# Optimization experiments

Hardware: AMD Instinct MI355X
Metric: run time of the kernel (lower is better)

The kernel has to match this reference:

```python
import jax, jax.numpy as jnp
import numpy as np

B, N, D, H, DH = 2, 4096, 256, 8, 64   # batch, nodes, dim, heads, dim_head
INNER = H * DH
POLY_K = 3  # polynomial order -> coeffs [H, POLY_K+1]
LN_EPS = 1e-5


def setup_inputs() -> dict:
    key = jax.random.key(0)
    ks = jax.random.split(key, 8)
    s = 0.02
    return {
        "x": jax.random.normal(ks[0], (B, N, D), dtype=jnp.float32),
        "Wq": jax.random.normal(ks[1], (D, INNER), dtype=jnp.float32) * s,
        "Wk": jax.random.normal(ks[2], (D, INNER), dtype=jnp.float32) * s,
        "Wv": jax.random.normal(ks[3], (D, INNER), dtype=jnp.float32) * s,
        "Wo": jax.random.normal(ks[4], (INNER, D), dtype=jnp.float32) * s,
        "gamma": jnp.ones((DH,), dtype=jnp.float32),
        "beta": jnp.zeros((DH,), dtype=jnp.float32),
        "coeffs": jax.random.normal(ks[5], (H, POLY_K + 1), dtype=jnp.float32) * 0.5,
    }


def reference(x, Wq, Wk, Wv, Wo, gamma, beta, coeffs):
    b, n, d = x.shape
    h, dh = coeffs.shape[0], gamma.shape[0]
    # --- graph estimator: per-head softmax adjacency A = softmax(QK^T/sqrt(dh)) ---
    q = (x @ Wq).reshape(b, n, h, dh).transpose(0, 2, 1, 3)  # bhnd
    k = (x @ Wk).reshape(b, n, h, dh).transpose(0, 2, 1, 3)  # bhnd
    scale = jax.lax.rsqrt(jnp.asarray(dh, x.dtype))
    A = jax.nn.softmax(jnp.einsum('bhnd,bhmd->bhnm', q, k) * scale, axis=-1)
    # --- value projection + per-head LayerNorm over dim_head ---
    v = (x @ Wv).reshape(b, n, h, dh)
    mu = v.mean(axis=-1, keepdims=True)
    var = ((v - mu) ** 2).mean(axis=-1, keepdims=True)
    v = (v - mu) * jax.lax.rsqrt(var + LN_EPS) * gamma + beta
    v = v.transpose(0, 2, 1, 3)  # bhnd
    # --- polynomial graph filter: y = sum_k c[h,k] * A^k v ---
    y = coeffs[None, :, 0, None, None] * v
    t = v
    for kk in range(1, coeffs.shape[1]):
        t = jnp.einsum('bhnm,bhmd->bhnd', A, t)
        y = y + coeffs[None, :, kk, None, None] * t
    # --- merge heads + output projection ---
    merged = y.transpose(0, 2, 1, 3).reshape(b, n, h * dh)
    return merged @ Wo
```

## Files before the change

kernel.cpp:

```cpp
#include <hip/hip_runtime.h>
#include <stdint.h>

#define B_ 2
#define N_ 4096
#define D_ 256
#define H_ 8
#define DH_ 64
#define INNER_ 512
#define NBH 16
#define PAD 72
#define FPAD 80

typedef unsigned short ushort_t;
typedef __attribute__((ext_vector_type(8))) short short8;
typedef __attribute__((ext_vector_type(4))) float float4v;
typedef __attribute__((ext_vector_type(4))) unsigned short ushort4v;
typedef __attribute__((ext_vector_type(4))) unsigned int uint4v;

__device__ __forceinline__ ushort_t f2bf(float f) {
    union { float f; unsigned int u; } v; v.f = f;
    unsigned int r = v.u + 0x7FFFu + ((v.u >> 16) & 1u);
    return (ushort_t)(r >> 16);
}
__device__ __forceinline__ float bf2f(ushort_t u) {
    union { unsigned int u; float f; } v; v.u = ((unsigned int)u) << 16;
    return v.f;
}
__device__ __forceinline__ unsigned char f2fp8s(float f) {
    union { float f; unsigned int u; } v; v.f = f;
    unsigned int s = (v.u >> 24) & 0x80u;
    v.u &= 0x7FFFFFFFu;
    float a = v.f;
    if (a >= 448.f) return (unsigned char)(s | 0x7E);
    if (a < 0.015625f) {
        int m = (int)(a * 512.f + 0.5f);
        return (unsigned char)(s | (unsigned)m);
    }
    unsigned int u = v.u + 0x7FFFFu + ((v.u >> 20) & 1u);
    return (unsigned char)(s | (((u >> 20) & 0x7FF) - 960));
}
__device__ __forceinline__ float fexp2(float x) {
    float r;
    asm volatile("v_exp_f32 %0, %1\n\ts_nop 0" : "=v"(r) : "v"(x));
    return r;
}

__global__ __launch_bounds__(256) void prep_kernel(
    const float* __restrict__ x, const float* __restrict__ Wq,
    const float* __restrict__ Wk, const float* __restrict__ Wv,
    const float* __restrict__ Wo,
    ushort_t* __restrict__ xb, ushort_t* __restrict__ WqkvT,
    ushort_t* __restrict__ WoT) {
    int idx = blockIdx.x * 256 + threadIdx.x;
    const int total_x = B_ * N_ * D_;
    const int total_wqkv = 3 * INNER_ * D_;
    const int total_wo = D_ * INNER_;
    if (idx < total_x) { xb[idx] = f2bf(x[idx]); return; }
    idx -= total_x;
    if (idx < total_wqkv) {
        int n = idx >> 8, k = idx & 255;
        int which = n >> 9, nn = n & 511;
        const float* W = (which == 0) ? Wq : ((which == 1) ? Wk : Wv);
        WqkvT[idx] = f2bf(W[k * INNER_ + nn]);
        return;
    }
    idx -= total_wqkv;
    if (idx < total_wo) {
        int c = idx >> 9, k = idx & 511;
        WoT[idx] = f2bf(Wo[k * D_ + c]);
    }
}

__global__ __launch_bounds__(256) void proj_gemm(
    const ushort_t* __restrict__ xb, const ushort_t* __restrict__ WqkvT,
    ushort_t* __restrict__ Qb, ushort_t* __restrict__ Kb,
    ushort_t* __restrict__ Vb) {
    __shared__ ushort_t As[128][PAD];
    __shared__ ushort_t Bs[128][PAD];
    int bid = blockIdx.x;
    int tileN = bid % 12, tileM = bid / 12;
    int tid = threadIdx.x;
    int w = tid >> 6, lane = tid & 63, q = lane >> 4, r = lane & 15;
    int wr = (w & 1) * 64, wc = (w >> 1) * 64;
    float4v acc[4][4];
    for (int i = 0; i < 4; i++)
        for (int j = 0; j < 4; j++)
            for (int e = 0; e < 4; e++) acc[i][j][e] = 0.f;

    for (int k0 = 0; k0 < 256; k0 += 64) {
        for (int it = 0; it < 4; it++) {
            int idx = tid + it * 256;
            int row = idx >> 3, kc = (idx & 7) * 8;
            *(short8*)&As[row][kc] =
                *(const short8*)&xb[(size_t)(tileM * 128 + row) * 256 + k0 + kc];
            *(short8*)&Bs[row][kc] =
                *(const short8*)&WqkvT[(size_t)(tileN * 128 + row) * 256 + k0 + kc];
        }
        __syncthreads();
        for (int kk = 0; kk < 64; kk += 32) {
            short8 a[4], b[4];
            for (int mi = 0; mi < 4; mi++)
                a[mi] = *(const short8*)&As[wr + mi * 16 + r][kk + q * 8];
            for (int ni = 0; ni < 4; ni++)
                b[ni] = *(const short8*)&Bs[wc + ni * 16 + r][kk + q * 8];
            for (int mi = 0; mi < 4; mi++)
                for (int ni = 0; ni < 4; ni++)
                    acc[mi][ni] = __builtin_amdgcn_mfma_f32_16x16x32_bf16(
                        a[mi], b[ni], acc[mi][ni], 0, 0, 0);
        }
        __syncthreads();
    }
    for (int mi = 0; mi < 4; mi++)
        for (int ni = 0; ni < 4; ni++)
            for (int reg = 0; reg < 4; reg++) {
                int grow = tileM * 128 + wr + mi * 16 + q * 4 + reg;
                int gcol = tileN * 128 + wc + ni * 16 + r;
                float v = acc[mi][ni][reg];
                int which = gcol >> 9, inner = gcol & 511;
                int h = inner >> 6, d = inner & 63;
                int b = grow >> 12, n = grow & 4095;
                size_t off = (((size_t)(b * H_ + h)) * N_ + n) * DH_ + d;
                if (which == 0) Qb[off] = f2bf(v * 0.18033688011112042f);
                else if (which == 1) Kb[off] = f2bf(v);
                else Vb[off] = f2bf(v);
            }
}

__global__ __launch_bounds__(256) void ln_kernel(
    const ushort_t* __restrict__ Vb, const float* __restrict__ gamma,
    const float* __restrict__ beta, const float* __restrict__ coeffs,
    unsigned char* __restrict__ t0T, float* __restrict__ y) {
    int tid = threadIdx.x;
    int wave = tid >> 6, lane = tid & 63;
    size_t row = (size_t)blockIdx.x * 4 + wave;
    int bh = (int)(row >> 12), n = (int)(row & 4095);
    int h = bh & 7;
    float v = bf2f(Vb[row * 64 + lane]);
    float s = v;
    for (int m = 32; m >= 1; m >>= 1) s += __shfl_xor(s, m, 64);
    float mu = s * (1.f / 64.f);
    float dv = v - mu;
    float s2 = dv * dv;
    for (int m = 32; m >= 1; m >>= 1) s2 += __shfl_xor(s2, m, 64);
    float var = s2 * (1.f / 64.f);
    float vln = dv * rsqrtf(var + 1e-5f) * gamma[lane] + beta[lane];
    float c0 = coeffs[h * 4 + 0];
    y[row * 64 + lane] = c0 * vln;
    t0T[((size_t)bh * 64 + lane) * 4096 + n] = f2fp8s(vln);
}


#define MFB(a, b, c) __builtin_amdgcn_mfma_f32_16x16x32_bf16(a, b, c, 0, 0, 0)
#define MFP(a, b, c) __builtin_amdgcn_mfma_f32_16x16x32_fp8_fp8(a, b, c, 0, 0, 0)

__device__ __forceinline__ long pk8(float4v x, float4v y) {
    int d0 = __builtin_amdgcn_cvt_pk_fp8_f32(fexp2(x[0]), fexp2(x[1]), 0, false);
    d0 = __builtin_amdgcn_cvt_pk_fp8_f32(fexp2(x[2]), fexp2(x[3]), d0, true);
    int d1 = __builtin_amdgcn_cvt_pk_fp8_f32(fexp2(y[0]), fexp2(y[1]), 0, false);
    d1 = __builtin_amdgcn_cvt_pk_fp8_f32(fexp2(y[2]), fexp2(y[3]), d1, true);
    return (long)(((unsigned long)(unsigned int)d1 << 32) | (unsigned int)d0);
}

#define WGBAR()                                                \
    do {                                                       \
        asm volatile("s_waitcnt lgkmcnt(0)" ::: "memory");     \
        __builtin_amdgcn_sched_barrier(0);                     \
        __builtin_amdgcn_s_barrier();                          \
        __builtin_amdgcn_sched_barrier(0);                     \
    } while (0)

#define COMPUTE32(KsX, TsX)                                                     \
    {                                                                           \
        short8 a0, a1;                                                          \
        float4v s00, s10, s20, s30, s01, s11, s21, s31;                         \
        a0 = *(const short8*)&KsX[r][q * 8];                                    \
        a1 = *(const short8*)&KsX[r][32 + q * 8];                               \
        s00 = MFB(a1, qf1, MFB(a0, qf0, zf));                                   \
        s01 = MFB(a1, qf3, MFB(a0, qf2, zf));                                   \
        a0 = *(const short8*)&KsX[16 + r][q * 8];                               \
        a1 = *(const short8*)&KsX[16 + r][32 + q * 8];                          \
        s10 = MFB(a1, qf1, MFB(a0, qf0, zf));                                   \
        s11 = MFB(a1, qf3, MFB(a0, qf2, zf));                                   \
        a0 = *(const short8*)&KsX[32 + r][q * 8];                               \
        a1 = *(const short8*)&KsX[32 + r][32 + q * 8];                          \
        s20 = MFB(a1, qf1, MFB(a0, qf0, zf));                                   \
        s21 = MFB(a1, qf3, MFB(a0, qf2, zf));                                   \
        a0 = *(const short8*)&KsX[48 + r][q * 8];                               \
        a1 = *(const short8*)&KsX[48 + r][32 + q * 8];                          \
        s30 = MFB(a1, qf1, MFB(a0, qf0, zf));                                   \
        s31 = MFB(a1, qf3, MFB(a0, qf2, zf));                                   \
        long eA0 = pk8(s00, s10), eB0 = pk8(s20, s30);                          \
        long eA1 = pk8(s01, s11), eB1 = pk8(s21, s31);                          \
        long b0 = *(const long*)&TsX[r][q * 8];                                 \
        long b1 = *(const long*)&TsX[16 + r][q * 8];                            \
        long b2 = *(const long*)&TsX[32 + r][q * 8];                            \
        long b3 = *(const long*)&TsX[48 + r][q * 8];                            \
        acc0[0] = MFP(eA0, b0, acc0[0]); acc1[0] = MFP(eA1, b0, acc1[0]);       \
        acc0[1] = MFP(eA0, b1, acc0[1]); acc1[1] = MFP(eA1, b1, acc1[1]);       \
        acc0[2] = MFP(eA0, b2, acc0[2]); acc1[2] = MFP(eA1, b2, acc1[2]);       \
        acc0[3] = MFP(eA0, b3, acc0[3]); acc1[3] = MFP(eA1, b3, acc1[3]);       \
        accs0 = MFP(eA0, bones, accs0);  accs1 = MFP(eA1, bones, accs1);        \
        b0 = *(const long*)&TsX[r][32 + q * 8];                                 \
        b1 = *(const long*)&TsX[16 + r][32 + q * 8];                            \
        b2 = *(const long*)&TsX[32 + r][32 + q * 8];                            \
        b3 = *(const long*)&TsX[48 + r][32 + q * 8];                            \
        acc0[0] = MFP(eB0, b0, acc0[0]); acc1[0] = MFP(eB1, b0, acc1[0]);       \
        acc0[1] = MFP(eB0, b1, acc0[1]); acc1[1] = MFP(eB1, b1, acc1[1]);       \
        acc0[2] = MFP(eB0, b2, acc0[2]); acc1[2] = MFP(eB1, b2, acc1[2]);       \
        acc0[3] = MFP(eB0, b3, acc0[3]); acc1[3] = MFP(eB1, b3, acc1[3]);       \
        accs0 = MFP(eB0, bones, accs0);  accs1 = MFP(eB1, bones, accs1);        \
    }

__global__ __launch_bounds__(512, 4) void poly_pass(
    const ushort_t* __restrict__ Qb, const ushort_t* __restrict__ Kb,
    const unsigned char* __restrict__ tinT, float* __restrict__ y,
    unsigned char* __restrict__ toutT, const float* __restrict__ coeffs,
    int kidx, int write_t) {
    __shared__ char smem[57344];
    typedef ushort_t KsArr[64][PAD];
    typedef unsigned char TsArr[64][FPAD];
    KsArr* Ks0 = (KsArr*)smem;
    KsArr* Ks1 = (KsArr*)(smem + 18432);
    TsArr* Ts0 = (TsArr*)(smem + 36864);
    TsArr* Ts1 = (TsArr*)(smem + 47104);

    int bid0 = blockIdx.x;
    int bid = ((bid0 & 7) << 6) | (bid0 >> 3);
    int bh = bid >> 5, ti = bid & 31;
    const ushort_t* Q = Qb + (size_t)bh * N_ * 64;
    const ushort_t* K = Kb + (size_t)bh * N_ * 64;
    const unsigned char* tin = tinT + (size_t)bh * 64 * N_;
    int tid = threadIdx.x, w = tid >> 6, lane = tid & 63, q = lane >> 4, r = lane & 15;
    int half = w >> 2, wsub = w & 3;
    const float4v zf = {0.f, 0.f, 0.f, 0.f};

    const ushort_t* qp = Q + (size_t)(ti * 128 + wsub * 32 + r) * 64 + q * 8;
    short8 qf0 = *(const short8*)qp;
    short8 qf1 = *(const short8*)(qp + 32);
    short8 qf2 = *(const short8*)(qp + 16 * 64);
    short8 qf3 = *(const short8*)(qp + 16 * 64 + 32);

    float4v acc0[4], acc1[4], accs0, accs1;
    for (int e = 0; e < 4; e++) { accs0[e] = 0.f; accs1[e] = 0.f; }
    for (int j = 0; j < 4; j++)
        for (int e = 0; e < 4; e++) { acc0[j][e] = 0.f; acc1[j][e] = 0.f; }
    const long bones = 0x3838383838383838L;

    int tl = tid & 255;
    int krow = tl >> 2, kpart = (tl & 3) * 16;
    int Lrow = (krow & 32) + ((krow & 4) << 2) + (krow & 3) + ((krow >> 3) & 3) * 4;
    const ushort_t* kp = K + (size_t)(half * 2048 + krow) * 64 + kpart;
    int srow = tl >> 2, scol = (tl & 3) * 16;
    const unsigned char* tp = tin + (size_t)srow * 4096 + half * 2048 + scol;

    {
        uint4v ka = *(const uint4v*)kp;
        uint4v kb = *(const uint4v*)(kp + 8);
        uint4v tv = *(const uint4v*)tp;
        *(uint4v*)&Ks0[half][Lrow][kpart] = ka;
        *(uint4v*)&Ks0[half][Lrow][kpart + 8] = kb;
        *(uint4v*)&Ts0[half][srow][scol] = tv;
    }
    uint4v pka = *(const uint4v*)(kp + 4096);
    uint4v pkb = *(const uint4v*)(kp + 4096 + 8);
    uint4v pt  = *(const uint4v*)(tp + 64);
    const ushort_t* kpl = kp + 2 * 4096;
    const unsigned char* tpl = tp + 2 * 64;
    WGBAR();

    for (int it = 0; it < 32; it += 2) {
        *(uint4v*)&Ks1[half][Lrow][kpart] = pka;
        *(uint4v*)&Ks1[half][Lrow][kpart + 8] = pkb;
        *(uint4v*)&Ts1[half][srow][scol] = pt;
        pka = *(const uint4v*)kpl;
        pkb = *(const uint4v*)(kpl + 8);
        pt  = *(const uint4v*)tpl;
        kpl += 4096; tpl += 64;
        COMPUTE32(Ks0[half], Ts0[half]);
        WGBAR();
        *(uint4v*)&Ks0[half][Lrow][kpart] = pka;
        *(uint4v*)&Ks0[half][Lrow][kpart + 8] = pkb;
        *(uint4v*)&Ts0[half][srow][scol] = pt;
        pka = *(const uint4v*)kpl;
        pkb = *(const uint4v*)(kpl + 8);
        pt  = *(const uint4v*)tpl;
        kpl += 4096; tpl += 64;
        COMPUTE32(Ks1[half], Ts1[half]);
        WGBAR();
    }

    float* ULDS = (float*)smem;
    unsigned char (*TT)[144] = (unsigned char(*)[144])(smem + 40960);

    if (half == 1) {
        float* ub = ULDS + (size_t)(wsub * 64 + lane) * 40;
#pragma unroll
        for (int j = 0; j < 4; j++) {
            *(float4v*)(ub + j * 4) = acc0[j];
            *(float4v*)(ub + 16 + j * 4) = acc1[j];
        }
        *(float4v*)(ub + 32) = accs0;
        *(float4v*)(ub + 36) = accs1;
    }
    WGBAR();
    if (half == 0) {
        const float* ub = ULDS + (size_t)(wsub * 64 + lane) * 40;
#pragma unroll
        for (int j = 0; j < 4; j++) {
            acc0[j] += *(const float4v*)(ub + j * 4);
            acc1[j] += *(const float4v*)(ub + 16 + j * 4);
        }
        accs0 += *(const float4v*)(ub + 32);
        accs1 += *(const float4v*)(ub + 36);

        int h = bh & 7;
        float ck = coeffs[h * 4 + kidx];
        float rinv0[4], rinv1[4];
#pragma unroll
        for (int reg = 0; reg < 4; reg++) {
            rinv0[reg] = 1.f / accs0[reg];
            rinv1[reg] = 1.f / accs1[reg];
        }
        float tv0[4][4], tv1[4][4];
#pragma unroll
        for (int ni = 0; ni < 4; ni++)
#pragma unroll
            for (int reg = 0; reg < 4; reg++) {
                tv0[ni][reg] = acc0[ni][reg] * rinv0[reg];
                tv1[ni][reg] = acc1[ni][reg] * rinv1[reg];
            }
#pragma unroll
        for (int reg = 0; reg < 4; reg++) {
            int il = wsub * 32 + q * 4 + reg;
            float* yp0 = y + ((size_t)bh * N_ + (size_t)ti * 128 + il) * 64;
            float* yp1 = yp0 + 16 * 64;
#pragma unroll
            for (int ni = 0; ni < 4; ni++) {
                yp0[ni * 16 + r] += ck * tv0[ni][reg];
                yp1[ni * 16 + r] += ck * tv1[ni][reg];
            }
        }
        if (write_t) {
#pragma unroll
            for (int ni = 0; ni < 4; ni++) {
                int p0 = __builtin_amdgcn_cvt_pk_fp8_f32(tv0[ni][0], tv0[ni][1], 0, false);
                p0 = __builtin_amdgcn_cvt_pk_fp8_f32(tv0[ni][2], tv0[ni][3], p0, true);
                *(unsigned int*)&TT[ni * 16 + r][wsub * 32 + q * 4] = (unsigned int)p0;
                int p1 = __builtin_amdgcn_cvt_pk_fp8_f32(tv1[ni][0], tv1[ni][1], 0, false);
                p1 = __builtin_amdgcn_cvt_pk_fp8_f32(tv1[ni][2], tv1[ni][3], p1, true);
                *(unsigned int*)&TT[ni * 16 + r][wsub * 32 + 16 + q * 4] = (unsigned int)p1;
            }
        }
    }
    if (write_t) {
        WGBAR();
        int drow = tid >> 3, dcol = (tid & 7) * 16;
        uint4v vv = *(const uint4v*)&TT[drow][dcol];
        *(uint4v*)&toutT[(size_t)bh * 64 * N_ + (size_t)drow * N_ + ti * 128 + dcol] = vv;
    }
}

__global__ __launch_bounds__(256) void out_gemm(
    const float* __restrict__ y, const ushort_t* __restrict__ WoT,
    float* __restrict__ out) {
    __shared__ ushort_t As[128][PAD];
    __shared__ ushort_t Bs[64][PAD];
    int bid = blockIdx.x;
    int tileN = bid & 3, tileM = bid >> 2;
    int tid = threadIdx.x, w = tid >> 6, lane = tid & 63, q = lane >> 4, r = lane & 15;
    int wr = w * 32;
    float4v acc[2][4];
    for (int i = 0; i < 2; i++)
        for (int j = 0; j < 4; j++)
            for (int e = 0; e < 4; e++) acc[i][j][e] = 0.f;

    for (int k0 = 0; k0 < 512; k0 += 64) {
        int h = k0 >> 6;
        for (int it = 0; it < 8; it++) {
            int idx = tid + it * 256;
            int row = idx >> 4, kc = (idx & 15) * 4;
            int grow = tileM * 128 + row;
            int b = grow >> 12, n = grow & 4095;
            const float4* src =
                (const float4*)&y[(((size_t)(b * H_ + h)) * N_ + n) * 64 + kc];
            float4 v = *src;
            ushort4v pv;
            pv[0] = f2bf(v.x); pv[1] = f2bf(v.y); pv[2] = f2bf(v.z); pv[3] = f2bf(v.w);
            *(ushort4v*)&As[row][kc] = pv;
        }
        for (int it = 0; it < 2; it++) {
            int idx = tid + it * 256;
            int row = idx >> 3, kc = (idx & 7) * 8;
            *(short8*)&Bs[row][kc] =
                *(const short8*)&WoT[(size_t)(tileN * 64 + row) * 512 + k0 + kc];
        }
        __syncthreads();
        for (int kk = 0; kk < 64; kk += 32) {
            short8 a[2], b[4];
            a[0] = *(const short8*)&As[wr + r][kk + q * 8];
            a[1] = *(const short8*)&As[wr + 16 + r][kk + q * 8];
            for (int ni = 0; ni < 4; ni++)
                b[ni] = *(const short8*)&Bs[ni * 16 + r][kk + q * 8];
            for (int mi = 0; mi < 2; mi++)
                for (int ni = 0; ni < 4; ni++)
                    acc[mi][ni] = __builtin_amdgcn_mfma_f32_16x16x32_bf16(
                        a[mi], b[ni], acc[mi][ni], 0, 0, 0);
        }
        __syncthreads();
    }
    for (int mi = 0; mi < 2; mi++)
        for (int reg = 0; reg < 4; reg++) {
            int grow = tileM * 128 + wr + mi * 16 + q * 4 + reg;
            for (int ni = 0; ni < 4; ni++) {
                int gcol = tileN * 64 + ni * 16 + r;
                out[(size_t)grow * 256 + gcol] = acc[mi][ni][reg];
            }
        }
}

extern "C" void kernel_launch(void* const* d_in, const int* in_sizes, int n_in,
                              void* d_out, int out_size, void* d_ws, size_t ws_size,
                              hipStream_t stream) {
    const float* x      = (const float*)d_in[0];
    const float* Wq     = (const float*)d_in[1];
    const float* Wk     = (const float*)d_in[2];
    const float* Wv     = (const float*)d_in[3];
    const float* Wo     = (const float*)d_in[4];
    const float* gamma  = (const float*)d_in[5];
    const float* beta   = (const float*)d_in[6];
    const float* coeffs = (const float*)d_in[7];
    float* out = (float*)d_out;

    char* ws = (char*)d_ws;
    size_t off = 0;
    auto alloc = [&](size_t bytes) -> void* {
        void* p = ws + off;
        off += (bytes + 255) & ~(size_t)255;
        return p;
    };
    ushort_t* xb    = (ushort_t*)alloc((size_t)B_ * N_ * D_ * 2);
    ushort_t* WqkvT = (ushort_t*)alloc((size_t)3 * INNER_ * D_ * 2);
    ushort_t* WoT   = (ushort_t*)alloc((size_t)D_ * INNER_ * 2);
    ushort_t* Qb    = (ushort_t*)alloc((size_t)NBH * N_ * DH_ * 2);
    ushort_t* Kb    = (ushort_t*)alloc((size_t)NBH * N_ * DH_ * 2);
    ushort_t* Vb    = (ushort_t*)alloc((size_t)NBH * N_ * DH_ * 2);
    unsigned char* t0T = (unsigned char*)alloc((size_t)NBH * DH_ * N_);
    unsigned char* t1T = (unsigned char*)alloc((size_t)NBH * DH_ * N_);
    float*    y     = (float*)alloc((size_t)NBH * N_ * DH_ * 4);

    const int prep_total = B_ * N_ * D_ + 3 * INNER_ * D_ + D_ * INNER_;
    prep_kernel<<<(prep_total + 255) / 256, 256, 0, stream>>>(
        x, Wq, Wk, Wv, Wo, xb, WqkvT, WoT);
    proj_gemm<<<768, 256, 0, stream>>>(xb, WqkvT, Qb, Kb, Vb);
    ln_kernel<<<(NBH * N_) / 4, 256, 0, stream>>>(Vb, gamma, beta, coeffs, t0T, y);

    poly_pass<<<NBH * 32, 512, 0, stream>>>(Qb, Kb, t0T, y, t1T, coeffs, 1, 1);
    poly_pass<<<NBH * 32, 512, 0, stream>>>(Qb, Kb, t1T, y, t0T, coeffs, 2, 1);
    poly_pass<<<NBH * 32, 512, 0, stream>>>(Qb, Kb, t0T, y, t1T, coeffs, 3, 0);

    out_gemm<<<256, 256, 0, stream>>>(y, WoT, out);
}
```

Baseline: 361.2 us.

## Double poly_pass query tile to 256 rows per block to reuse K/T tiles

Each poly_pass block now handles 256 query rows (64 per wave) instead of 128. Each K and T tile loaded into LDS therefore feeds twice as many MFMAs, which halves the number of blocks and the global and LDS traffic per unit of work. The cost is roughly double the accumulator registers per wave, so launch bounds drop to 2 waves-per-EU, and only 256 blocks are launched, which may leave the 256 CUs underfilled. LDS padding changes and the split-K reduction across wave halves now runs in two rounds to fit the larger accumulators.

```diff
diff --git a/kernel.cpp b/kernel.cpp
--- a/kernel.cpp
+++ b/kernel.cpp
@@ -9,7 +9,8 @@
 #define INNER_ 512
 #define NBH 16
 #define PAD 72
-#define FPAD 80
+#define KPAD 74
+#define FPAD 88
 
 typedef unsigned short ushort_t;
 typedef __attribute__((ext_vector_type(8))) short short8;
@@ -169,64 +170,91 @@
         __builtin_amdgcn_sched_barrier(0);                     \
     } while (0)
 
-#define COMPUTE32(KsX, TsX)                                                     \
+#define COMPUTE64(KsX, TsX)                                                     \
     {                                                                           \
         short8 a0, a1;                                                          \
-        float4v s00, s10, s20, s30, s01, s11, s21, s31;                         \
-        a0 = *(const short8*)&KsX[r][q * 8];                                    \
-        a1 = *(const short8*)&KsX[r][32 + q * 8];                               \
-        s00 = MFB(a1, qf1, MFB(a0, qf0, zf));                                   \
-        s01 = MFB(a1, qf3, MFB(a0, qf2, zf));                                   \
-        a0 = *(const short8*)&KsX[16 + r][q * 8];                               \
-        a1 = *(const short8*)&KsX[16 + r][32 + q * 8];                          \
-        s10 = MFB(a1, qf1, MFB(a0, qf0, zf));                                   \
-        s11 = MFB(a1, qf3, MFB(a0, qf2, zf));                                   \
-        a0 = *(const short8*)&KsX[32 + r][q * 8];                               \
-        a1 = *(const short8*)&KsX[32 + r][32 + q * 8];                          \
-        s20 = MFB(a1, qf1, MFB(a0, qf0, zf));                                   \
-        s21 = MFB(a1, qf3, MFB(a0, qf2, zf));                                   \
-        a0 = *(const short8*)&KsX[48 + r][q * 8];                               \
-        a1 = *(const short8*)&KsX[48 + r][32 + q * 8];                          \
-        s30 = MFB(a1, qf1, MFB(a0, qf0, zf));                                   \
-        s31 = MFB(a1, qf3, MFB(a0, qf2, zf));                                   \
-        long eA0 = pk8(s00, s10), eB0 = pk8(s20, s30);                          \
-        long eA1 = pk8(s01, s11), eB1 = pk8(s21, s31);                          \
-        long b0 = *(const long*)&TsX[r][q * 8];                                 \
-        long b1 = *(const long*)&TsX[16 + r][q * 8];                            \
-        long b2 = *(const long*)&TsX[32 + r][q * 8];                            \
-        long b3 = *(const long*)&TsX[48 + r][q * 8];                            \
-        acc0[0] = MFP(eA0, b0, acc0[0]); acc1[0] = MFP(eA1, b0, acc1[0]);       \
-        acc0[1] = MFP(eA0, b1, acc0[1]); acc1[1] = MFP(eA1, b1, acc1[1]);       \
-        acc0[2] = MFP(eA0, b2, acc0[2]); acc1[2] = MFP(eA1, b2, acc1[2]);       \
-        acc0[3] = MFP(eA0, b3, acc0[3]); acc1[3] = MFP(eA1, b3, acc1[3]);       \
-        accs0 = MFP(eA0, bones, accs0);  accs1 = MFP(eA1, bones, accs1);        \
-        b0 = *(const long*)&TsX[r][32 + q * 8];                                 \
-        b1 = *(const long*)&TsX[16 + r][32 + q * 8];                            \
-        b2 = *(const long*)&TsX[32 + r][32 + q * 8];                            \
-        b3 = *(const long*)&TsX[48 + r][32 + q * 8];                            \
-        acc0[0] = MFP(eB0, b0, acc0[0]); acc1[0] = MFP(eB1, b0, acc1[0]);       \
-        acc0[1] = MFP(eB0, b1, acc0[1]); acc1[1] = MFP(eB1, b1, acc1[1]);       \
-        acc0[2] = MFP(eB0, b2, acc0[2]); acc1[2] = MFP(eB1, b2, acc1[2]);       \
-        acc0[3] = MFP(eB0, b3, acc0[3]); acc1[3] = MFP(eB1, b3, acc1[3]);       \
-        accs0 = MFP(eB0, bones, accs0);  accs1 = MFP(eB1, bones, accs1);        \
-    }
-
-__global__ __launch_bounds__(512, 4) void poly_pass(
+        long e00, e01, e02, e03, e10, e11, e12, e13;                            \
+        {                                                                       \
+            float4v sA0, sA1, sA2, sA3, sB0, sB1, sB2, sB3;                     \
+            a0 = *(const short8*)&KsX[r][q * 8];                                \
+            a1 = *(const short8*)&KsX[r][32 + q * 8];                           \
+            sA0 = MFB(a1, qf0b, MFB(a0, qf0a, zf));                             \
+            sA1 = MFB(a1, qf1b, MFB(a0, qf1a, zf));                             \
+            sA2 = MFB(a1, qf2b, MFB(a0, qf2a, zf));                             \
+            sA3 = MFB(a1, qf3b, MFB(a0, qf3a, zf));                             \
+            a0 = *(const short8*)&KsX[16 + r][q * 8];                           \
+            a1 = *(const short8*)&KsX[16 + r][32 + q * 8];                      \
+            sB0 = MFB(a1, qf0b, MFB(a0, qf0a, zf));                             \
+            sB1 = MFB(a1, qf1b, MFB(a0, qf1a, zf));                             \
+            sB2 = MFB(a1, qf2b, MFB(a0, qf2a, zf));                             \
+            sB3 = MFB(a1, qf3b, MFB(a0, qf3a, zf));                             \
+            e00 = pk8(sA0, sB0); e01 = pk8(sA1, sB1);                           \
+            e02 = pk8(sA2, sB2); e03 = pk8(sA3, sB3);                           \
+        }                                                                       \
+        {                                                                       \
+            float4v sA0, sA1, sA2, sA3, sB0, sB1, sB2, sB3;                     \
+            a0 = *(const short8*)&KsX[32 + r][q * 8];                           \
+            a1 = *(const short8*)&KsX[32 + r][32 + q * 8];                      \
+            sA0 = MFB(a1, qf0b, MFB(a0, qf0a, zf));                             \
+            sA1 = MFB(a1, qf1b, MFB(a0, qf1a, zf));                             \
+            sA2 = MFB(a1, qf2b, MFB(a0, qf2a, zf));                             \
+            sA3 = MFB(a1, qf3b, MFB(a0, qf3a, zf));                             \
+            a0 = *(const short8*)&KsX[48 + r][q * 8];                           \
+            a1 = *(const short8*)&KsX[48 + r][32 + q * 8];                      \
+            sB0 = MFB(a1, qf0b, MFB(a0, qf0a, zf));                             \
+            sB1 = MFB(a1, qf1b, MFB(a0, qf1a, zf));                             \
+            sB2 = MFB(a1, qf2b, MFB(a0, qf2a, zf));                             \
+            sB3 = MFB(a1, qf3b, MFB(a0, qf3a, zf));                             \
+            e10 = pk8(sA0, sB0); e11 = pk8(sA1, sB1);                           \
+            e12 = pk8(sA2, sB2); e13 = pk8(sA3, sB3);                           \
+        }                                                                       \
+        long tb;                                                                \
+        tb = *(const long*)&TsX[r][q * 8];                                      \
+        acc0[0] = MFP(e00, tb, acc0[0]); acc1[0] = MFP(e01, tb, acc1[0]);       \
+        acc2[0] = MFP(e02, tb, acc2[0]); acc3[0] = MFP(e03, tb, acc3[0]);       \
+        tb = *(const long*)&TsX[r][32 + q * 8];                                 \
+        acc0[0] = MFP(e10, tb, acc0[0]); acc1[0] = MFP(e11, tb, acc1[0]);       \
+        acc2[0] = MFP(e12, tb, acc2[0]); acc3[0] = MFP(e13, tb, acc3[0]);       \
+        tb = *(const long*)&TsX[16 + r][q * 8];                                 \
+        acc0[1] = MFP(e00, tb, acc0[1]); acc1[1] = MFP(e01, tb, acc1[1]);       \
+        acc2[1] = MFP(e02, tb, acc2[1]); acc3[1] = MFP(e03, tb, acc3[1]);       \
+        tb = *(const long*)&TsX[16 + r][32 + q * 8];                            \
+        acc0[1] = MFP(e10, tb, acc0[1]); acc1[1] = MFP(e11, tb, acc1[1]);       \
+        acc2[1] = MFP(e12, tb, acc2[1]); acc3[1] = MFP(e13, tb, acc3[1]);       \
+        tb = *(const long*)&TsX[32 + r][q * 8];                                 \
+        acc0[2] = MFP(e00, tb, acc0[2]); acc1[2] = MFP(e01, tb, acc1[2]);       \
+        acc2[2] = MFP(e02, tb, acc2[2]); acc3[2] = MFP(e03, tb, acc3[2]);       \
+        tb = *(const long*)&TsX[32 + r][32 + q * 8];                            \
+        acc0[2] = MFP(e10, tb, acc0[2]); acc1[2] = MFP(e11, tb, acc1[2]);       \
+        acc2[2] = MFP(e12, tb, acc2[2]); acc3[2] = MFP(e13, tb, acc3[2]);       \
+        tb = *(const long*)&TsX[48 + r][q * 8];                                 \
+        acc0[3] = MFP(e00, tb, acc0[3]); acc1[3] = MFP(e01, tb, acc1[3]);       \
+        acc2[3] = MFP(e02, tb, acc2[3]); acc3[3] = MFP(e03, tb, acc3[3]);       \
+        tb = *(const long*)&TsX[48 + r][32 + q * 8];                            \
+        acc0[3] = MFP(e10, tb, acc0[3]); acc1[3] = MFP(e11, tb, acc1[3]);       \
+        acc2[3] = MFP(e12, tb, acc2[3]); acc3[3] = MFP(e13, tb, acc3[3]);       \
+        accs0 = MFP(e00, bones, accs0); accs0 = MFP(e10, bones, accs0);         \
+        accs1 = MFP(e01, bones, accs1); accs1 = MFP(e11, bones, accs1);         \
+        accs2 = MFP(e02, bones, accs2); accs2 = MFP(e12, bones, accs2);         \
+        accs3 = MFP(e03, bones, accs3); accs3 = MFP(e13, bones, accs3);         \
+    }
+
+__global__ __launch_bounds__(512, 2) void poly_pass(
     const ushort_t* __restrict__ Qb, const ushort_t* __restrict__ Kb,
     const unsigned char* __restrict__ tinT, float* __restrict__ y,
     unsigned char* __restrict__ toutT, const float* __restrict__ coeffs,
     int kidx, int write_t) {
-    __shared__ char smem[57344];
-    typedef ushort_t KsArr[64][PAD];
+    __shared__ char smem[60416];
+    typedef ushort_t KsArr[64][KPAD];
     typedef unsigned char TsArr[64][FPAD];
     KsArr* Ks0 = (KsArr*)smem;
-    KsArr* Ks1 = (KsArr*)(smem + 18432);
-    TsArr* Ts0 = (TsArr*)(smem + 36864);
-    TsArr* Ts1 = (TsArr*)(smem + 47104);
+    KsArr* Ks1 = (KsArr*)(smem + 18944);
+    TsArr* Ts0 = (TsArr*)(smem + 37888);
+    TsArr* Ts1 = (TsArr*)(smem + 49152);
 
     int bid0 = blockIdx.x;
-    int bid = ((bid0 & 7) << 6) | (bid0 >> 3);
-    int bh = bid >> 5, ti = bid & 31;
+    int bid = ((bid0 & 7) << 5) | (bid0 >> 3);
+    int bh = bid >> 4, ti = bid & 15;
     const ushort_t* Q = Qb + (size_t)bh * N_ * 64;
     const ushort_t* K = Kb + (size_t)bh * N_ * 64;
     const unsigned char* tin = tinT + (size_t)bh * 64 * N_;
@@ -234,16 +262,20 @@
     int half = w >> 2, wsub = w & 3;
     const float4v zf = {0.f, 0.f, 0.f, 0.f};
 
-    const ushort_t* qp = Q + (size_t)(ti * 128 + wsub * 32 + r) * 64 + q * 8;
-    short8 qf0 = *(const short8*)qp;
-    short8 qf1 = *(const short8*)(qp + 32);
-    short8 qf2 = *(const short8*)(qp + 16 * 64);
-    short8 qf3 = *(const short8*)(qp + 16 * 64 + 32);
-
-    float4v acc0[4], acc1[4], accs0, accs1;
-    for (int e = 0; e < 4; e++) { accs0[e] = 0.f; accs1[e] = 0.f; }
+    const ushort_t* qp = Q + (size_t)(ti * 256 + wsub * 64 + r) * 64 + q * 8;
+    short8 qf0a = *(const short8*)qp;
+    short8 qf0b = *(const short8*)(qp + 32);
+    short8 qf1a = *(const short8*)(qp + 16 * 64);
+    short8 qf1b = *(const short8*)(qp + 16 * 64 + 32);
+    short8 qf2a = *(const short8*)(qp + 32 * 64);
+    short8 qf2b = *(const short8*)(qp + 32 * 64 + 32);
+    short8 qf3a = *(const short8*)(qp + 48 * 64);
+    short8 qf3b = *(const short8*)(qp + 48 * 64 + 32);
+
+    float4v acc0[4], acc1[4], acc2[4], acc3[4], accs0, accs1, accs2, accs3;
+    for (int e = 0; e < 4; e++) { accs0[e] = 0.f; accs1[e] = 0.f; accs2[e] = 0.f; accs3[e] = 0.f; }
     for (int j = 0; j < 4; j++)
-        for (int e = 0; e < 4; e++) { acc0[j][e] = 0.f; acc1[j][e] = 0.f; }
+        for (int e = 0; e < 4; e++) { acc0[j][e] = 0.f; acc1[j][e] = 0.f; acc2[j][e] = 0.f; acc3[j][e] = 0.f; }
     const long bones = 0x3838383838383838L;
 
     int tl = tid & 255;
@@ -276,7 +308,7 @@
         pkb = *(const uint4v*)(kpl + 8);
         pt  = *(const uint4v*)tpl;
         kpl += 4096; tpl += 64;
-        COMPUTE32(Ks0[half], Ts0[half]);
+        COMPUTE64(Ks0[half], Ts0[half]);
         WGBAR();
         *(uint4v*)&Ks0[half][Lrow][kpart] = pka;
         *(uint4v*)&Ks0[half][Lrow][kpart + 8] = pkb;
@@ -285,78 +317,105 @@
         pkb = *(const uint4v*)(kpl + 8);
         pt  = *(const uint4v*)tpl;
         kpl += 4096; tpl += 64;
-        COMPUTE32(Ks1[half], Ts1[half]);
+        COMPUTE64(Ks1[half], Ts1[half]);
         WGBAR();
     }
 
     float* ULDS = (float*)smem;
-    unsigned char (*TT)[144] = (unsigned char(*)[144])(smem + 40960);
-
-    if (half == 1) {
-        float* ub = ULDS + (size_t)(wsub * 64 + lane) * 40;
-#pragma unroll
-        for (int j = 0; j < 4; j++) {
-            *(float4v*)(ub + j * 4) = acc0[j];
-            *(float4v*)(ub + 16 + j * 4) = acc1[j];
-        }
-        *(float4v*)(ub + 32) = accs0;
-        *(float4v*)(ub + 36) = accs1;
-    }
-    WGBAR();
+    for (int rr = 0; rr < 2; rr++) {
+        if (half == 1 && (wsub >> 1) == rr) {
+            float* ub = ULDS + (size_t)((wsub & 1) * 64 + lane) * 84;
+            *(float4v*)(ub + 0)  = acc0[0]; *(float4v*)(ub + 4)  = acc0[1];
+            *(float4v*)(ub + 8)  = acc0[2]; *(float4v*)(ub + 12) = acc0[3];
+            *(float4v*)(ub + 16) = acc1[0]; *(float4v*)(ub + 20) = acc1[1];
+            *(float4v*)(ub + 24) = acc1[2]; *(float4v*)(ub + 28) = acc1[3];
+            *(float4v*)(ub + 32) = acc2[0]; *(float4v*)(ub + 36) = acc2[1];
+            *(float4v*)(ub + 40) = acc2[2]; *(float4v*)(ub + 44) = acc2[3];
+            *(float4v*)(ub + 48) = acc3[0]; *(float4v*)(ub + 52) = acc3[1];
+            *(float4v*)(ub + 56) = acc3[2]; *(float4v*)(ub + 60) = acc3[3];
+            *(float4v*)(ub + 64) = accs0;   *(float4v*)(ub + 68) = accs1;
+            *(float4v*)(ub + 72) = accs2;   *(float4v*)(ub + 76) = accs3;
+        }
+        WGBAR();
+        if (half == 0 && (wsub >> 1) == rr) {
+            const float* ub = ULDS + (size_t)((wsub & 1) * 64 + lane) * 84;
+            acc0[0] += *(const float4v*)(ub + 0);  acc0[1] += *(const float4v*)(ub + 4);
+            acc0[2] += *(const float4v*)(ub + 8);  acc0[3] += *(const float4v*)(ub + 12);
+            acc1[0] += *(const float4v*)(ub + 16); acc1[1] += *(const float4v*)(ub + 20);
+            acc1[2] += *(const float4v*)(ub + 24); acc1[3] += *(const float4v*)(ub + 28);
+            acc2[0] += *(const float4v*)(ub + 32); acc2[1] += *(const float4v*)(ub + 36);
+            acc2[2] += *(const float4v*)(ub + 40); acc2[3] += *(const float4v*)(ub + 44);
+            acc3[0] += *(const float4v*)(ub + 48); acc3[1] += *(const float4v*)(ub + 52);
+            acc3[2] += *(const float4v*)(ub + 56); acc3[3] += *(const float4v*)(ub + 60);
+            accs0 += *(const float4v*)(ub + 64);   accs1 += *(const float4v*)(ub + 68);
+            accs2 += *(const float4v*)(ub + 72);   accs3 += *(const float4v*)(ub + 76);
+        }
+        WGBAR();
+    }
+
+    unsigned char (*TT)[272] = (unsigned char(*)[272])smem;
     if (half == 0) {
-        const float* ub = ULDS + (size_t)(wsub * 64 + lane) * 40;
-#pragma unroll
-        for (int j = 0; j < 4; j++) {
-            acc0[j] += *(const float4v*)(ub + j * 4);
-            acc1[j] += *(const float4v*)(ub + 16 + j * 4);
-        }
-        accs0 += *(const float4v*)(ub + 32);
-        accs1 += *(const float4v*)(ub + 36);
-
         int h = bh & 7;
         float ck = coeffs[h * 4 + kidx];
-        float rinv0[4], rinv1[4];
+        float r0[4], r1[4], r2[4], r3[4];
 #pragma unroll
         for (int reg = 0; reg < 4; reg++) {
-            rinv0[reg] = 1.f / accs0[reg];
-            rinv1[reg] = 1.f / accs1[reg];
-        }
-        float tv0[4][4], tv1[4][4];
+            r0[reg] = 1.f / accs0[reg]; r1[reg] = 1.f / accs1[reg];
+            r2[reg] = 1.f / accs2[reg]; r3[reg] = 1.f / accs3[reg];
+        }
+        float tv0[4][4], tv1[4][4], tv2[4][4], tv3[4][4];
 #pragma unroll
-        for (int ni = 0; ni < 4; ni++)
+        for (int dg = 0; dg < 4; dg++)
 #pragma unroll
             for (int reg = 0; reg < 4; reg++) {
-                tv0[ni][reg] = acc0[ni][reg] * rinv0[reg];
-                tv1[ni][reg] = acc1[ni][reg] * rinv1[reg];
+                tv0[dg][reg] = acc0[dg][reg] * r0[reg];
+                tv1[dg][reg] = acc1[dg][reg] * r1[reg];
+                tv2[dg][reg] = acc2[dg][reg] * r2[reg];
+                tv3[dg][reg] = acc3[dg][reg] * r3[reg];
             }
 #pragma unroll
         for (int reg = 0; reg < 4; reg++) {
-            int il = wsub * 32 + q * 4 + reg;
-            float* yp0 = y + ((size_t)bh * N_ + (size_t)ti * 128 + il) * 64;
-            float* yp1 = yp0 + 16 * 64;
+            size_t ibase = (size_t)bh * N_ + (size_t)ti * 256 + wsub * 64 + q * 4 + reg;
+            float* yp0 = y + (ibase + 0)  * 64;
+            float* yp1 = y + (ibase + 16) * 64;
+            float* yp2 = y + (ibase + 32) * 64;
+            float* yp3 = y + (ibase + 48) * 64;
 #pragma unroll
-            for (int ni = 0; ni < 4; ni++) {
-                yp0[ni * 16 + r] += ck * tv0[ni][reg];
-                yp1[ni * 16 + r] += ck * tv1[ni][reg];
+            for (int dg = 0; dg < 4; dg++) {
+                yp0[dg * 16 + r] += ck * tv0[dg][reg];
+                yp1[dg * 16 + r] += ck * tv1[dg][reg];
+                yp2[dg * 16 + r] += ck * tv2[dg][reg];
+                yp3[dg * 16 + r] += ck * tv3[dg][reg];
             }
         }
         if (write_t) {
 #pragma unroll
-            for (int ni = 0; ni < 4; ni++) {
-                int p0 = __builtin_amdgcn_cvt_pk_fp8_f32(tv0[ni][0], tv0[ni][1], 0, false);
-                p0 = __builtin_amdgcn_cvt_pk_fp8_f32(tv0[ni][2], tv0[ni][3], p0, true);
-                *(unsigned int*)&TT[ni * 16 + r][wsub * 32 + q * 4] = (unsigned int)p0;
-                int p1 = __builtin_amdgcn_cvt_pk_fp8_f32(tv1[ni][0], tv1[ni][1], 0, false);
-                p1 = __builtin_amdgcn_cvt_pk_fp8_f32(tv1[ni][2], tv1[ni][3], p1, true);
-                *(unsigned int*)&TT[ni * 16 + r][wsub * 32 + 16 + q * 4] = (unsigned int)p1;
+            for (int dg = 0; dg < 4; dg++) {
+                int p;
+                p = __builtin_amdgcn_cvt_pk_fp8_f32(tv0[dg][0], tv0[dg][1], 0, false);
+                p = __builtin_amdgcn_cvt_pk_fp8_f32(tv0[dg][2], tv0[dg][3], p, true);
+                *(unsigned int*)&TT[dg * 16 + r][wsub * 64 + q * 4] = (unsigned int)p;
+                p = __builtin_amdgcn_cvt_pk_fp8_f32(tv1[dg][0], tv1[dg][1], 0, false);
+                p = __builtin_amdgcn_cvt_pk_fp8_f32(tv1[dg][2], tv1[dg][3], p, true);
+                *(unsigned int*)&TT[dg * 16 + r][wsub * 64 + 16 + q * 4] = (unsigned int)p;
+                p = __builtin_amdgcn_cvt_pk_fp8_f32(tv2[dg][0], tv2[dg][1], 0, false);
+                p = __builtin_amdgcn_cvt_pk_fp8_f32(tv2[dg][2], tv2[dg][3], p, true);
+                *(unsigned int*)&TT[dg * 16 + r][wsub * 64 + 32 + q * 4] = (unsigned int)p;
+                p = __builtin_amdgcn_cvt_pk_fp8_f32(tv3[dg][0], tv3[dg][1], 0, false);
+                p = __builtin_amdgcn_cvt_pk_fp8_f32(tv3[dg][2], tv3[dg][3], p, true);
+                *(unsigned int*)&TT[dg * 16 + r][wsub * 64 + 48 + q * 4] = (unsigned int)p;
             }
         }
     }
     if (write_t) {
         WGBAR();
-        int drow = tid >> 3, dcol = (tid & 7) * 16;
-        uint4v vv = *(const uint4v*)&TT[drow][dcol];
-        *(uint4v*)&toutT[(size_t)bh * 64 * N_ + (size_t)drow * N_ + ti * 128 + dcol] = vv;
+        int drow = tid >> 3, dcol = (tid & 7) * 32;
+        uint4v v0 = *(const uint4v*)&TT[drow][dcol];
+        uint4v v1 = *(const uint4v*)&TT[drow][dcol + 16];
+        unsigned char* dst =
+            toutT + (size_t)bh * 64 * N_ + (size_t)drow * N_ + ti * 256 + dcol;
+        *(uint4v*)dst = v0;
+        *(uint4v*)(dst + 16) = v1;
     }
 }
 
@@ -454,9 +513,9 @@
     proj_gemm<<<768, 256, 0, stream>>>(xb, WqkvT, Qb, Kb, Vb);
     ln_kernel<<<(NBH * N_) / 4, 256, 0, stream>>>(Vb, gamma, beta, coeffs, t0T, y);
 
-    poly_pass<<<NBH * 32, 512, 0, stream>>>(Qb, Kb, t0T, y, t1T, coeffs, 1, 1);
-    poly_pass<<<NBH * 32, 512, 0, stream>>>(Qb, Kb, t1T, y, t0T, coeffs, 2, 1);
-    poly_pass<<<NBH * 32, 512, 0, stream>>>(Qb, Kb, t0T, y, t1T, coeffs, 3, 0);
+    poly_pass<<<NBH * 16, 512, 0, stream>>>(Qb, Kb, t0T, y, t1T, coeffs, 1, 1);
+    poly_pass<<<NBH * 16, 512, 0, stream>>>(Qb, Kb, t1T, y, t0T, coeffs, 2, 1);
+    poly_pass<<<NBH * 16, 512, 0, stream>>>(Qb, Kb, t0T, y, t1T, coeffs, 3, 0);
 
     out_gemm<<<256, 256, 0, stream>>>(y, WoT, out);
 }
```

Measured after the change: 517.7 us. 43.3% more time.
